# Kernel optimization log

Hardware: AMD Instinct MI355X
Metric: run time of the kernel (lower is better)

Reference implementation:

```python
import jax, jax.numpy as jnp
import numpy as np

SYNCNET_T = 5
EMB_D = 512


def _l2norm(x, eps=1e-12):
    return x / jnp.maximum(jnp.linalg.norm(x, axis=-1, keepdims=True), eps)


def setup_inputs() -> dict:
    key = jax.random.key(0)
    k = jax.random.split(key, 6)
    b = 256
    a_1 = jax.random.normal(k[0], (b, 1, 80, 16), dtype=jnp.float32)
    a_2 = jax.random.normal(k[1], (b, 1, 80, 16), dtype=jnp.float32)
    v_1 = jax.random.normal(k[2], (b, 3, SYNCNET_T, 96, 96), dtype=jnp.float32)
    v_2 = jax.random.normal(k[3], (b, 3, SYNCNET_T, 96, 96), dtype=jnp.float32)
    da = 1 * 80 * 16
    dv = 3 * SYNCNET_T * 48 * 96
    W_a = jax.random.normal(k[4], (da, EMB_D), dtype=jnp.float32) / np.float32(np.sqrt(da))
    W_v = jax.random.normal(k[5], (dv, EMB_D), dtype=jnp.float32) / np.float32(np.sqrt(dv))
    return {"a_1": a_1, "v_1": v_1, "a_2": a_2, "v_2": v_2, "W_a": W_a, "W_v": W_v}


def reference(a_1, v_1, a_2, v_2, W_a, W_v):
    b = a_1.shape[0]
    audio = jnp.concatenate([a_1, a_2], axis=0)      # (2b,1,80,16)
    visual = jnp.concatenate([v_1, v_2], axis=0)     # (2b,3,T,96,96)
    visual = visual[:, :, :, visual.shape[3] // 2:]  # lower half -> (2b,3,T,48,96)
    # torch.cat([visual[:,:,i] for i in range(T)], dim=1) -> channel order (T,3)
    n2 = visual.shape[0]
    visual = jnp.moveaxis(visual, 2, 1).reshape(n2, 3 * SYNCNET_T, 48, 96)
    # syncnet (modeled): flatten -> linear -> L2 normalize, 512-d embeddings
    a = _l2norm(audio.reshape(n2, -1) @ W_a)  # (2b,d)
    v = _l2norm(visual.reshape(n2, -1) @ W_v)  # (2b,d)
    a1, a2 = a[:b], a[b:]
    v1, v2 = v[:b], v[b:]
    dot = lambda x, y: jnp.sum(x * y, axis=-1)
    # numerator: product of {a1,a2}x{v1,v2} + combos within audio and within visual
    numerator = (jnp.exp(dot(a1, v1)) + jnp.exp(dot(a1, v2))
                 + jnp.exp(dot(a2, v1)) + jnp.exp(dot(a2, v2))
                 + jnp.exp(dot(a1, a2)) + jnp.exp(dot(v1, v2)))  # (b,)
    # denominator: product of {a1,a2} with ALL visual embeddings v (2b)
    denominator = (jnp.exp(a1 @ v.T) + jnp.exp(a2 @ v.T)).sum(axis=1)  # (b,)
    loss = -jnp.mean(jnp.log(numerator / denominator))
    return loss
```

## Files before the change

kernel.cpp:

```cpp
#include <hip/hip_runtime.h>

typedef __attribute__((ext_vector_type(8))) short bf16x8;
typedef __attribute__((ext_vector_type(4))) float f32x4;
typedef __attribute__((ext_vector_type(2))) unsigned int u32x2;

#define KSV 45
#define KSA 2

__device__ __forceinline__ unsigned int pk2(float a, float b) {
    unsigned int r;
    asm("v_cvt_pk_bf16_f32 %0, %1, %2" : "=v"(r) : "v"(a), "v"(b));
    return r;
}

__device__ __forceinline__ u32x2 tr_lo(unsigned addr) {
    u32x2 r;
    asm volatile("ds_read_b64_tr_b16 %0, %1" : "=v"(r) : "v"(addr));
    return r;
}
__device__ __forceinline__ u32x2 tr_hi(unsigned addr) {
    u32x2 r;
    asm volatile("ds_read_b64_tr_b16 %0, %1 offset:1024" : "=v"(r) : "v"(addr));
    return r;
}

template<int CROP>
__global__ __launch_bounds__(256, 2) void gemm_kernel(
    const float* __restrict__ s1, const float* __restrict__ s2,
    const float* __restrict__ W, float* __restrict__ part, int ksteps)
{
    __shared__ uint4 As[512];
    __shared__ uint4 Bs[512];

    const int tid = threadIdx.x;
    const int blk = blockIdx.x;
    const int cpx = gridDim.x >> 3;
    const int lin = (blk & 7) * cpx + (blk >> 3);
    const int z  = lin >> 4;
    const int mn = lin & 15;
    const int m0 = (mn >> 2) * 128;
    const int n0 = (mn & 3) * 128;
    const int k0 = z * ksteps * 32;
    part += (size_t)z * 262144;

    const int a_row = tid >> 1;
    const int a_off = (tid & 1) << 4;
    const int grow  = m0 + a_row;
    const int ROWSTR = CROP ? 138240 : 1280;
    const float* abase = (grow < 256) ? s1 + (size_t)grow * ROWSTR
                                      : s2 + (size_t)(grow - 256) * ROWSTR;
    const int a_u0 = a_row * 4 + (((tid & 1) * 2 + 0) ^ (a_row & 3));
    const int a_u1 = a_row * 4 + (((tid & 1) * 2 + 1) ^ (a_row & 3));

    const int b_k = tid >> 3;
    const int b_g = tid & 7;
    const float* bbase = W + (size_t)b_k * 512 + b_g * 16;
    const int b_u0 = (b_k >> 2) * 64 + b_g * 8 + (b_k & 3) * 2;

    const int lane = tid & 63;
    const int wid  = tid >> 6;
    const int l15  = lane & 15;
    const int lk   = lane >> 4;
    const int wm = (wid >> 1) * 64;
    const int wn = (wid & 1) * 64;

    int ua[4];
    #pragma unroll
    for (int mi = 0; mi < 4; ++mi) {
        const int row = wm + mi * 16 + l15;
        ua[mi] = row * 4 + (lk ^ (row & 3));
    }
    const unsigned bsBase = (unsigned)(uintptr_t)(void*)(&Bs[0]);
    unsigned btr[4];
    #pragma unroll
    for (int ni = 0; ni < 4; ++ni)
        btr[ni] = bsBase + (unsigned)((2 * lk) * 1024 + ((wn >> 4) + ni) * 128 + l15 * 2);

    f32x4 acc[4][4];
    #pragma unroll
    for (int mi = 0; mi < 4; ++mi)
        #pragma unroll
        for (int ni = 0; ni < 4; ++ni) acc[mi][ni] = f32x4{0.f, 0.f, 0.f, 0.f};

    auto LOADA = [&](f32x4* av, int ks) {
        const int kgs = k0 + ks * 32;
        const float* ap;
        if (CROP) {
            const int p = kgs / 4608;
            const int j = kgs - p * 4608;
            const int c = p % 3, t9 = p / 3;
            ap = abase + c * 46080 + t9 * 9216 + 4608 + j + a_off;
        } else {
            ap = abase + kgs + a_off;
        }
        #pragma unroll
        for (int i = 0; i < 4; ++i) av[i] = *(const f32x4*)(ap + 4 * i);
    };
    auto LOADB = [&](f32x4* bv, int ks) {
        const float* bp = bbase + (size_t)(k0 + ks * 32) * 512;
        #pragma unroll
        for (int i = 0; i < 4; ++i) bv[i] = *(const f32x4*)(bp + 4 * i);
    };
    auto PACK = [&](const f32x4* av, const f32x4* bv) {
        uint4 pa0, pa1, pb0, pb1;
        pa0.x = pk2(av[0].x, av[0].y); pa0.y = pk2(av[0].z, av[0].w);
        pa0.z = pk2(av[1].x, av[1].y); pa0.w = pk2(av[1].z, av[1].w);
        pa1.x = pk2(av[2].x, av[2].y); pa1.y = pk2(av[2].z, av[2].w);
        pa1.z = pk2(av[3].x, av[3].y); pa1.w = pk2(av[3].z, av[3].w);
        As[a_u0] = pa0;
        As[a_u1] = pa1;
        pb0.x = pk2(bv[0].x, bv[0].y); pb0.y = pk2(bv[0].z, bv[0].w);
        pb0.z = pk2(bv[1].x, bv[1].y); pb0.w = pk2(bv[1].z, bv[1].w);
        pb1.x = pk2(bv[2].x, bv[2].y); pb1.y = pk2(bv[2].z, bv[2].w);
        pb1.z = pk2(bv[3].x, bv[3].y); pb1.w = pk2(bv[3].z, bv[3].w);
        Bs[b_u0]     = pb0;
        Bs[b_u0 + 1] = pb1;
    };
    auto COMPUTE = [&]() {
        bf16x8 af[4];
        #pragma unroll
        for (int mi = 0; mi < 4; ++mi) af[mi] = __builtin_bit_cast(bf16x8, As[ua[mi]]);
        u32x2 lo[4], hi[4];
        #pragma unroll
        for (int ni = 0; ni < 4; ++ni) { lo[ni] = tr_lo(btr[ni]); hi[ni] = tr_hi(btr[ni]); }
        asm volatile("s_waitcnt lgkmcnt(0)" ::: "memory");
        __builtin_amdgcn_sched_barrier(0);
        bf16x8 bf[4];
        #pragma unroll
        for (int ni = 0; ni < 4; ++ni) {
            uint4 q; q.x = lo[ni].x; q.y = lo[ni].y; q.z = hi[ni].x; q.w = hi[ni].y;
            bf[ni] = __builtin_bit_cast(bf16x8, q);
        }
        #pragma unroll
        for (int mi = 0; mi < 4; ++mi)
            #pragma unroll
            for (int ni = 0; ni < 4; ++ni)
                acc[mi][ni] = __builtin_amdgcn_mfma_f32_16x16x32_bf16(af[mi], bf[ni], acc[mi][ni], 0, 0, 0);
    };

    f32x4 av0[4], bv0[4], av1[4], bv1[4];
    LOADA(av0, 0); LOADB(bv0, 0);
    for (int ks = 0; ks < ksteps; ks += 2) {
        LOADA(av1, ks + 1); LOADB(bv1, ks + 1);
        PACK(av0, bv0);
        __syncthreads();
        COMPUTE();
        __syncthreads();
        if (ks + 2 < ksteps) { LOADA(av0, ks + 2); LOADB(bv0, ks + 2); }
        PACK(av1, bv1);
        __syncthreads();
        COMPUTE();
        __syncthreads();
    }

    #pragma unroll
    for (int mi = 0; mi < 4; ++mi)
        #pragma unroll
        for (int ni = 0; ni < 4; ++ni) {
            const int col = n0 + wn + ni * 16 + l15;
            #pragma unroll
            for (int r = 0; r < 4; ++r) {
                const int row = m0 + wm + mi * 16 + lk * 4 + r;
                part[(size_t)row * 512 + col] = acc[mi][ni][r];
            }
        }
}

__global__ __launch_bounds__(256) void norm_kernel(
    const float* __restrict__ partA, const float* __restrict__ partV,
    float* __restrict__ Aout, float* __restrict__ Vout, int nzV)
{
    const int row = blockIdx.x;
    const int tid = threadIdx.x;
    const bool isV = row >= 512;
    const int r = isV ? (row - 512) : row;
    const int c0 = tid, c1 = tid + 256;

    float v0 = 0.f, v1 = 0.f;
    if (isV) {
        for (int zz = 0; zz < nzV; ++zz) {
            const float* p = partV + (size_t)zz * 262144 + (size_t)r * 512;
            v0 += p[c0]; v1 += p[c1];
        }
    } else {
        #pragma unroll
        for (int zz = 0; zz < KSA; ++zz) {
            const float* p = partA + (size_t)zz * 262144 + (size_t)r * 512;
            v0 += p[c0]; v1 += p[c1];
        }
    }

    float ss = v0 * v0 + v1 * v1;
    #pragma unroll
    for (int off = 32; off > 0; off >>= 1) ss += __shfl_down(ss, off);
    __shared__ float sbuf[4];
    if ((tid & 63) == 0) sbuf[tid >> 6] = ss;
    __syncthreads();
    const float total = sbuf[0] + sbuf[1] + sbuf[2] + sbuf[3];
    const float inv = 1.f / fmaxf(sqrtf(total), 1e-12f);

    float* outp = (isV ? Vout : Aout) + (size_t)r * 512;
    outp[c0] = v0 * inv;
    outp[c1] = v1 * inv;
}

__global__ __launch_bounds__(256) void sim_kernel(
    const float* __restrict__ A, const float* __restrict__ V,
    float* __restrict__ den, float* __restrict__ num)
{
    __shared__ uint4 As[2][256];
    __shared__ uint4 Bs[2][256];

    const int tid = threadIdx.x;
    const int m0 = (blockIdx.x >> 3) * 64;
    const int n0 = (blockIdx.x & 7) * 64;
    const int nsteps = 16;

    const int a_row = tid >> 2, a_kb = tid & 3;
    const int b_col = tid & 63, b_kb = tid >> 6;
    const int a_u = (a_kb * 64 + a_row) ^ (a_kb << 1);
    const int b_u = (b_kb * 64 + b_col) ^ (b_kb << 1);

    const float* abase = A + (size_t)(m0 + a_row) * 512;
    const float* bptr  = V + (size_t)(n0 + b_col) * 512 + b_kb * 8;
    int aoff = a_kb * 8;

    const int lane = tid & 63, wid = tid >> 6;
    const int wrow = (wid >> 1) * 32, wcol = (wid & 1) * 32;
    const int l15 = lane & 15, lk = lane >> 4;

    int ra[2], rb[2];
    #pragma unroll
    for (int m = 0; m < 2; ++m) ra[m] = (lk * 64 + wrow + m * 16 + l15) ^ (lk << 1);
    #pragma unroll
    for (int n = 0; n < 2; ++n) rb[n] = (lk * 64 + wcol + n * 16 + l15) ^ (lk << 1);

    f32x4 acc[2][2];
    #pragma unroll
    for (int m = 0; m < 2; ++m)
        #pragma unroll
        for (int n = 0; n < 2; ++n) acc[m][n] = f32x4{0.f, 0.f, 0.f, 0.f};

    float4 A0 = *(const float4*)(abase + aoff);
    float4 A1 = *(const float4*)(abase + aoff + 4);
    float4 B0 = *(const float4*)bptr;
    float4 B1 = *(const float4*)(bptr + 4);

    for (int ks = 0; ks < nsteps; ++ks) {
        const int cur = ks & 1;
        const bool more = (ks + 1 < nsteps);
        float4 A0n, A1n, B0n, B1n;
        if (more) {
            aoff += 32; bptr += 32;
            A0n = *(const float4*)(abase + aoff);
            A1n = *(const float4*)(abase + aoff + 4);
            B0n = *(const float4*)bptr;
            B1n = *(const float4*)(bptr + 4);
        }
        uint4 pa;
        pa.x = pk2(A0.x, A0.y); pa.y = pk2(A0.z, A0.w);
        pa.z = pk2(A1.x, A1.y); pa.w = pk2(A1.z, A1.w);
        As[cur][a_u] = pa;
        uint4 pb;
        pb.x = pk2(B0.x, B0.y); pb.y = pk2(B0.z, B0.w);
        pb.z = pk2(B1.x, B1.y); pb.w = pk2(B1.z, B1.w);
        Bs[cur][b_u] = pb;
        __syncthreads();

        bf16x8 af[2], bfr[2];
        #pragma unroll
        for (int m = 0; m < 2; ++m) af[m] = __builtin_bit_cast(bf16x8, As[cur][ra[m]]);
        #pragma unroll
        for (int n = 0; n < 2; ++n) bfr[n] = __builtin_bit_cast(bf16x8, Bs[cur][rb[n]]);
        #pragma unroll
        for (int m = 0; m < 2; ++m)
            #pragma unroll
            for (int n = 0; n < 2; ++n)
                acc[m][n] = __builtin_amdgcn_mfma_f32_16x16x32_bf16(af[m], bfr[n], acc[m][n], 0, 0, 0);

        if (more) { A0 = A0n; A1 = A1n; B0 = B0n; B1 = B1n; }
    }

    #pragma unroll
    for (int m = 0; m < 2; ++m) {
        float rs[4] = {0.f, 0.f, 0.f, 0.f};
        #pragma unroll
        for (int n = 0; n < 2; ++n) {
            const int col = n0 + wcol + n * 16 + l15;
            #pragma unroll
            for (int r = 0; r < 4; ++r) {
                const int row = m0 + wrow + m * 16 + lk * 4 + r;
                const float e = __expf(acc[m][n][r]);
                rs[r] += e;
                if (((row - col) & 255) == 0) atomicAdd(num + (row & 255), e);
            }
        }
        #pragma unroll
        for (int r = 0; r < 4; ++r) {
            float v = rs[r];
            v += __shfl_xor(v, 1);
            v += __shfl_xor(v, 2);
            v += __shfl_xor(v, 4);
            v += __shfl_xor(v, 8);
            if (l15 == 0) {
                const int row = m0 + wrow + m * 16 + lk * 4 + r;
                atomicAdd(den + (row & 255), v);
            }
        }
    }
}

__global__ __launch_bounds__(512) void zero_kernel(float* __restrict__ p) {
    p[threadIdx.x] = 0.f;
}

__global__ __launch_bounds__(256) void dots_kernel(
    const float* __restrict__ A, const float* __restrict__ V,
    float* __restrict__ num)
{
    const int b = blockIdx.x;
    const int i = b & 255;
    const float* X = (b < 256) ? A : V;
    const float* x = X + (size_t)i * 512;
    const float* y = X + (size_t)(i + 256) * 512;
    const int tid = threadIdx.x;
    float d = x[tid] * y[tid] + x[tid + 256] * y[tid + 256];
    #pragma unroll
    for (int off = 32; off > 0; off >>= 1) d += __shfl_down(d, off);
    __shared__ float sbuf[4];
    if ((tid & 63) == 0) sbuf[tid >> 6] = d;
    __syncthreads();
    if (tid == 0) atomicAdd(num + i, __expf(sbuf[0] + sbuf[1] + sbuf[2] + sbuf[3]));
}

__global__ __launch_bounds__(256) void final_kernel(
    const float* __restrict__ den, const float* __restrict__ num,
    float* __restrict__ out)
{
    const int tid = threadIdx.x;
    float v = logf(den[tid]) - logf(num[tid]);
    #pragma unroll
    for (int off = 32; off > 0; off >>= 1) v += __shfl_down(v, off);
    __shared__ float sbuf[4];
    if ((tid & 63) == 0) sbuf[tid >> 6] = v;
    __syncthreads();
    if (tid == 0) out[0] = (sbuf[0] + sbuf[1] + sbuf[2] + sbuf[3]) * (1.f / 256.f);
}

extern "C" void kernel_launch(void* const* d_in, const int* in_sizes, int n_in,
                              void* d_out, int out_size, void* d_ws, size_t ws_size,
                              hipStream_t stream)
{
    (void)in_sizes; (void)n_in; (void)out_size; (void)ws_size;
    const float* a_1 = (const float*)d_in[0];
    const float* v_1 = (const float*)d_in[1];
    const float* a_2 = (const float*)d_in[2];
    const float* v_2 = (const float*)d_in[3];
    const float* W_a = (const float*)d_in[4];
    const float* W_v = (const float*)d_in[5];
    float* out = (float*)d_out;

    float* cur   = (float*)d_ws;
    float* den   = cur; cur += 256;
    float* num   = cur; cur += 256;
    float* Anorm = cur; cur += 262144;
    float* Vnorm = cur; cur += 262144;
    float* partA = cur; cur += (size_t)KSA * 262144;
    float* partV = cur; cur += (size_t)KSV * 262144;

    zero_kernel<<<1, 512, 0, stream>>>(den);

    gemm_kernel<1><<<16 * KSV, 256, 0, stream>>>(v_1, v_2, W_v, partV, 48);
    gemm_kernel<0><<<16 * KSA, 256, 0, stream>>>(a_1, a_2, W_a, partA, 20);

    norm_kernel<<<1024, 256, 0, stream>>>(partA, partV, Anorm, Vnorm, KSV);
    sim_kernel<<<64, 256, 0, stream>>>(Anorm, Vnorm, den, num);
    dots_kernel<<<512, 256, 0, stream>>>(Anorm, Vnorm, num);
    final_kernel<<<1, 256, 0, stream>>>(den, num, out);
}
```

Before: 189.3 us.

## Rework split-K GEMM to 256x256 tiles with 512 threads and padded LDS

Replaces the 128x128 split-K GEMM with 256x256 output tiles per block, using 512 threads, 8 waves each computing 128x64. Split-K depth changes from 45 to 72 chunks. The B operand is loaded as dword pairs and packed transposed into a padded 80-byte-stride LDS layout, so the transposed-read instructions are no longer needed. The loop becomes a single-buffered pipeline using inline-asm global loads with explicit waitcnt and barriers. The larger tiles cut redundant reads of the fp32 activations and weights, but they raise register pressure, need more LDS, and write more split-K partials for the norm kernel to reduce.

```diff
diff --git a/kernel.cpp b/kernel.cpp
--- a/kernel.cpp
+++ b/kernel.cpp
@@ -2,159 +2,158 @@
 
 typedef __attribute__((ext_vector_type(8))) short bf16x8;
 typedef __attribute__((ext_vector_type(4))) float f32x4;
-typedef __attribute__((ext_vector_type(2))) unsigned int u32x2;
-
-#define KSV 45
-#define KSA 2
+typedef __attribute__((ext_vector_type(2))) float f32x2;
+
+#define ZV 72
+#define ZA 2
 
 __device__ __forceinline__ unsigned int pk2(float a, float b) {
     unsigned int r;
     asm("v_cvt_pk_bf16_f32 %0, %1, %2" : "=v"(r) : "v"(a), "v"(b));
     return r;
 }
-
-__device__ __forceinline__ u32x2 tr_lo(unsigned addr) {
-    u32x2 r;
-    asm volatile("ds_read_b64_tr_b16 %0, %1" : "=v"(r) : "v"(addr));
-    return r;
-}
-__device__ __forceinline__ u32x2 tr_hi(unsigned addr) {
-    u32x2 r;
-    asm volatile("ds_read_b64_tr_b16 %0, %1 offset:1024" : "=v"(r) : "v"(addr));
-    return r;
+__device__ __forceinline__ void gl4_0 (f32x4& d, const float* p) { asm volatile("global_load_dwordx4 %0, %1, off"            : "=&v"(d) : "v"(p)); }
+__device__ __forceinline__ void gl4_16(f32x4& d, const float* p) { asm volatile("global_load_dwordx4 %0, %1, off offset:16"  : "=&v"(d) : "v"(p)); }
+__device__ __forceinline__ void gl4_32(f32x4& d, const float* p) { asm volatile("global_load_dwordx4 %0, %1, off offset:32"  : "=&v"(d) : "v"(p)); }
+__device__ __forceinline__ void gl4_48(f32x4& d, const float* p) { asm volatile("global_load_dwordx4 %0, %1, off offset:48"  : "=&v"(d) : "v"(p)); }
+__device__ __forceinline__ void gl2_0 (f32x2& d, const float* p) { asm volatile("global_load_dwordx2 %0, %1, off"            : "=&v"(d) : "v"(p)); }
+__device__ __forceinline__ void gl2_2k(f32x2& d, const float* p) { asm volatile("global_load_dwordx2 %0, %1, off offset:2048": "=&v"(d) : "v"(p)); }
+
+__device__ __forceinline__ void waitv0() {
+    asm volatile("s_waitcnt vmcnt(0)" ::: "memory");
+    __builtin_amdgcn_sched_barrier(0);
+}
+__device__ __forceinline__ void barrier_lgkm() {
+    asm volatile("s_waitcnt lgkmcnt(0)" ::: "memory");
+    __builtin_amdgcn_sched_barrier(0);
+    __builtin_amdgcn_s_barrier();
+    __builtin_amdgcn_sched_barrier(0);
+}
+__device__ __forceinline__ void barrier_only() {
+    __builtin_amdgcn_sched_barrier(0);
+    __builtin_amdgcn_s_barrier();
+    __builtin_amdgcn_sched_barrier(0);
 }
 
 template<int CROP>
-__global__ __launch_bounds__(256, 2) void gemm_kernel(
+__global__ __launch_bounds__(512, 2) void fgemm(
     const float* __restrict__ s1, const float* __restrict__ s2,
-    const float* __restrict__ W, float* __restrict__ part, int ksteps)
-{
-    __shared__ uint4 As[512];
-    __shared__ uint4 Bs[512];
+    const float* __restrict__ W, float* __restrict__ part, int nsteps)
+{
+    __shared__ unsigned char lds[40960];
+    unsigned char* Asb = lds;
+    unsigned char* Bsb = lds + 20480;
 
     const int tid = threadIdx.x;
     const int blk = blockIdx.x;
     const int cpx = gridDim.x >> 3;
     const int lin = (blk & 7) * cpx + (blk >> 3);
-    const int z  = lin >> 4;
-    const int mn = lin & 15;
-    const int m0 = (mn >> 2) * 128;
-    const int n0 = (mn & 3) * 128;
-    const int k0 = z * ksteps * 32;
+    const int z    = lin >> 2;
+    const int tile = lin & 3;
+    const int m0 = (tile >> 1) * 256;
+    const int n0 = (tile & 1) * 256;
+    const int k0 = z * nsteps * 32;
     part += (size_t)z * 262144;
 
-    const int a_row = tid >> 1;
-    const int a_off = (tid & 1) << 4;
-    const int grow  = m0 + a_row;
+    const int a_row  = tid >> 1;
+    const int a_half = tid & 1;
+    const int grow = m0 + a_row;
     const int ROWSTR = CROP ? 138240 : 1280;
-    const float* abase = (grow < 256) ? s1 + (size_t)grow * ROWSTR
-                                      : s2 + (size_t)(grow - 256) * ROWSTR;
-    const int a_u0 = a_row * 4 + (((tid & 1) * 2 + 0) ^ (a_row & 3));
-    const int a_u1 = a_row * 4 + (((tid & 1) * 2 + 1) ^ (a_row & 3));
-
-    const int b_k = tid >> 3;
-    const int b_g = tid & 7;
-    const float* bbase = W + (size_t)b_k * 512 + b_g * 16;
-    const int b_u0 = (b_k >> 2) * 64 + b_g * 8 + (b_k & 3) * 2;
-
-    const int lane = tid & 63;
-    const int wid  = tid >> 6;
-    const int l15  = lane & 15;
-    const int lk   = lane >> 4;
-    const int wm = (wid >> 1) * 64;
-    const int wn = (wid & 1) * 64;
-
-    int ua[4];
-    #pragma unroll
-    for (int mi = 0; mi < 4; ++mi) {
-        const int row = wm + mi * 16 + l15;
-        ua[mi] = row * 4 + (lk ^ (row & 3));
-    }
-    const unsigned bsBase = (unsigned)(uintptr_t)(void*)(&Bs[0]);
-    unsigned btr[4];
+    const float* abase0 = (grow < 256) ? s1 + (size_t)grow * ROWSTR
+                                       : s2 + (size_t)(grow - 256) * ROWSTR;
+    const float* abase = abase0 + a_half * 16;
+
+    const int b_np  = tid >> 2;
+    const int b_oct = tid & 3;
+    const float* bb0 = W + (size_t)(k0 + b_oct * 8) * 512 + n0 + 2 * b_np;
+    const float* bb1 = bb0 + 1024;
+    const float* bb2 = bb0 + 2048;
+    const float* bb3 = bb0 + 3072;
+
+    const int lane = tid & 63, wid = tid >> 6;
+    const int l15 = lane & 15, lk = lane >> 4;
+    const int wm = (wid >> 2) * 128;
+    const int wn = (wid & 3) * 64;
+
+    const unsigned char* arp[8];
+    #pragma unroll
+    for (int mi = 0; mi < 8; ++mi)
+        arp[mi] = Asb + (wm + mi * 16 + l15) * 80 + lk * 16;
+    const unsigned char* brp[4];
     #pragma unroll
     for (int ni = 0; ni < 4; ++ni)
-        btr[ni] = bsBase + (unsigned)((2 * lk) * 1024 + ((wn >> 4) + ni) * 128 + l15 * 2);
-
-    f32x4 acc[4][4];
-    #pragma unroll
-    for (int mi = 0; mi < 4; ++mi)
+        brp[ni] = Bsb + (wn + ni * 16 + l15) * 80 + lk * 16;
+
+    f32x4 acc[8][4];
+    #pragma unroll
+    for (int mi = 0; mi < 8; ++mi)
         #pragma unroll
         for (int ni = 0; ni < 4; ++ni) acc[mi][ni] = f32x4{0.f, 0.f, 0.f, 0.f};
 
-    auto LOADA = [&](f32x4* av, int ks) {
-        const int kgs = k0 + ks * 32;
+    f32x4 av[4];
+    f32x2 bv[8];
+    int kgs = k0;
+
+    auto ISSUE = [&]() {
         const float* ap;
         if (CROP) {
             const int p = kgs / 4608;
             const int j = kgs - p * 4608;
-            const int c = p % 3, t9 = p / 3;
-            ap = abase + c * 46080 + t9 * 9216 + 4608 + j + a_off;
+            const int c3 = p % 3, t9 = p / 3;
+            ap = abase + c3 * 46080 + t9 * 9216 + 4608 + j;
         } else {
-            ap = abase + kgs + a_off;
-        }
-        #pragma unroll
-        for (int i = 0; i < 4; ++i) av[i] = *(const f32x4*)(ap + 4 * i);
+            ap = abase + kgs;
+        }
+        gl4_0(av[0], ap); gl4_16(av[1], ap); gl4_32(av[2], ap); gl4_48(av[3], ap);
+        gl2_0(bv[0], bb0); gl2_2k(bv[1], bb0);
+        gl2_0(bv[2], bb1); gl2_2k(bv[3], bb1);
+        gl2_0(bv[4], bb2); gl2_2k(bv[5], bb2);
+        gl2_0(bv[6], bb3); gl2_2k(bv[7], bb3);
     };
-    auto LOADB = [&](f32x4* bv, int ks) {
-        const float* bp = bbase + (size_t)(k0 + ks * 32) * 512;
-        #pragma unroll
-        for (int i = 0; i < 4; ++i) bv[i] = *(const f32x4*)(bp + 4 * i);
+    auto ADV = [&]() {
+        kgs += 32;
+        bb0 += 16384; bb1 += 16384; bb2 += 16384; bb3 += 16384;
     };
-    auto PACK = [&](const f32x4* av, const f32x4* bv) {
-        uint4 pa0, pa1, pb0, pb1;
-        pa0.x = pk2(av[0].x, av[0].y); pa0.y = pk2(av[0].z, av[0].w);
-        pa0.z = pk2(av[1].x, av[1].y); pa0.w = pk2(av[1].z, av[1].w);
-        pa1.x = pk2(av[2].x, av[2].y); pa1.y = pk2(av[2].z, av[2].w);
-        pa1.z = pk2(av[3].x, av[3].y); pa1.w = pk2(av[3].z, av[3].w);
-        As[a_u0] = pa0;
-        As[a_u1] = pa1;
-        pb0.x = pk2(bv[0].x, bv[0].y); pb0.y = pk2(bv[0].z, bv[0].w);
-        pb0.z = pk2(bv[1].x, bv[1].y); pb0.w = pk2(bv[1].z, bv[1].w);
-        pb1.x = pk2(bv[2].x, bv[2].y); pb1.y = pk2(bv[2].z, bv[2].w);
-        pb1.z = pk2(bv[3].x, bv[3].y); pb1.w = pk2(bv[3].z, bv[3].w);
-        Bs[b_u0]     = pb0;
-        Bs[b_u0 + 1] = pb1;
+    auto PACK = [&]() {
+        uint4 w0, w1;
+        w0.x = pk2(av[0].x, av[0].y); w0.y = pk2(av[0].z, av[0].w);
+        w0.z = pk2(av[1].x, av[1].y); w0.w = pk2(av[1].z, av[1].w);
+        w1.x = pk2(av[2].x, av[2].y); w1.y = pk2(av[2].z, av[2].w);
+        w1.z = pk2(av[3].x, av[3].y); w1.w = pk2(av[3].z, av[3].w);
+        *(uint4*)(Asb + a_row * 80 + a_half * 32)      = w0;
+        *(uint4*)(Asb + a_row * 80 + a_half * 32 + 16) = w1;
+        uint4 bx, by;
+        bx.x = pk2(bv[0].x, bv[1].x); bx.y = pk2(bv[2].x, bv[3].x);
+        bx.z = pk2(bv[4].x, bv[5].x); bx.w = pk2(bv[6].x, bv[7].x);
+        by.x = pk2(bv[0].y, bv[1].y); by.y = pk2(bv[2].y, bv[3].y);
+        by.z = pk2(bv[4].y, bv[5].y); by.w = pk2(bv[6].y, bv[7].y);
+        *(uint4*)(Bsb + (2 * b_np) * 80 + b_oct * 16)     = bx;
+        *(uint4*)(Bsb + (2 * b_np + 1) * 80 + b_oct * 16) = by;
     };
-    auto COMPUTE = [&]() {
-        bf16x8 af[4];
-        #pragma unroll
-        for (int mi = 0; mi < 4; ++mi) af[mi] = __builtin_bit_cast(bf16x8, As[ua[mi]]);
-        u32x2 lo[4], hi[4];
-        #pragma unroll
-        for (int ni = 0; ni < 4; ++ni) { lo[ni] = tr_lo(btr[ni]); hi[ni] = tr_hi(btr[ni]); }
-        asm volatile("s_waitcnt lgkmcnt(0)" ::: "memory");
-        __builtin_amdgcn_sched_barrier(0);
-        bf16x8 bf[4];
-        #pragma unroll
-        for (int ni = 0; ni < 4; ++ni) {
-            uint4 q; q.x = lo[ni].x; q.y = lo[ni].y; q.z = hi[ni].x; q.w = hi[ni].y;
-            bf[ni] = __builtin_bit_cast(bf16x8, q);
-        }
-        #pragma unroll
-        for (int mi = 0; mi < 4; ++mi)
+
+    ISSUE();
+    for (int ks = 0; ks < nsteps; ++ks) {
+        waitv0();
+        PACK();
+        if (ks + 1 < nsteps) { ADV(); ISSUE(); }
+        barrier_lgkm();
+
+        bf16x8 af[8], bf[4];
+        #pragma unroll
+        for (int mi = 0; mi < 8; ++mi) af[mi] = __builtin_bit_cast(bf16x8, *(const uint4*)arp[mi]);
+        #pragma unroll
+        for (int ni = 0; ni < 4; ++ni) bf[ni] = __builtin_bit_cast(bf16x8, *(const uint4*)brp[ni]);
+        #pragma unroll
+        for (int mi = 0; mi < 8; ++mi)
             #pragma unroll
             for (int ni = 0; ni < 4; ++ni)
                 acc[mi][ni] = __builtin_amdgcn_mfma_f32_16x16x32_bf16(af[mi], bf[ni], acc[mi][ni], 0, 0, 0);
-    };
-
-    f32x4 av0[4], bv0[4], av1[4], bv1[4];
-    LOADA(av0, 0); LOADB(bv0, 0);
-    for (int ks = 0; ks < ksteps; ks += 2) {
-        LOADA(av1, ks + 1); LOADB(bv1, ks + 1);
-        PACK(av0, bv0);
-        __syncthreads();
-        COMPUTE();
-        __syncthreads();
-        if (ks + 2 < ksteps) { LOADA(av0, ks + 2); LOADB(bv0, ks + 2); }
-        PACK(av1, bv1);
-        __syncthreads();
-        COMPUTE();
-        __syncthreads();
+
+        barrier_only();
     }
 
     #pragma unroll
-    for (int mi = 0; mi < 4; ++mi)
+    for (int mi = 0; mi < 8; ++mi)
         #pragma unroll
         for (int ni = 0; ni < 4; ++ni) {
             const int col = n0 + wn + ni * 16 + l15;
@@ -184,7 +183,7 @@
         }
     } else {
         #pragma unroll
-        for (int zz = 0; zz < KSA; ++zz) {
+        for (int zz = 0; zz < ZA; ++zz) {
             const float* p = partA + (size_t)zz * 262144 + (size_t)r * 512;
             v0 += p[c0]; v1 += p[c1];
         }
@@ -365,15 +364,15 @@
     float* num   = cur; cur += 256;
     float* Anorm = cur; cur += 262144;
     float* Vnorm = cur; cur += 262144;
-    float* partA = cur; cur += (size_t)KSA * 262144;
-    float* partV = cur; cur += (size_t)KSV * 262144;
+    float* partA = cur; cur += (size_t)ZA * 262144;
+    float* partV = cur; cur += (size_t)ZV * 262144;
 
     zero_kernel<<<1, 512, 0, stream>>>(den);
 
-    gemm_kernel<1><<<16 * KSV, 256, 0, stream>>>(v_1, v_2, W_v, partV, 48);
-    gemm_kernel<0><<<16 * KSA, 256, 0, stream>>>(a_1, a_2, W_a, partA, 20);
-
-    norm_kernel<<<1024, 256, 0, stream>>>(partA, partV, Anorm, Vnorm, KSV);
+    fgemm<1><<<4 * ZV, 512, 0, stream>>>(v_1, v_2, W_v, partV, 30);
+    fgemm<0><<<4 * ZA, 512, 0, stream>>>(a_1, a_2, W_a, partA, 20);
+
+    norm_kernel<<<1024, 256, 0, stream>>>(partA, partV, Anorm, Vnorm, ZV);
     sim_kernel<<<64, 256, 0, stream>>>(Anorm, Vnorm, den, num);
     dots_kernel<<<512, 256, 0, stream>>>(Anorm, Vnorm, num);
     final_kernel<<<1, 256, 0, stream>>>(den, num, out);
```

Measured after the change: 249.0 us. +31.5%, slower.
